# Kernel optimization log

Measured on AMD Instinct MI355X. Metric: run time of the kernel, lower is better.

The kernel has to match this reference:

```python
import jax, jax.numpy as jnp
import numpy as np

H, W = 200, 200           # BEV spatial shape (single level)
NBQ, NH, NL, NP = 2, 8, 1, 4
D = 256
HD = D // NH


def setup_inputs() -> dict:
    key = jax.random.key(0)
    ks = jax.random.split(key, 12)
    bs, nq = 1, H * W
    query = jax.random.normal(ks[0], (bs, nq, D), jnp.float32)
    value = jax.random.normal(ks[1], (bs, NBQ * nq, D), jnp.float32)
    reference_points = jax.random.uniform(ks[2], (bs, nq, NL, 2), dtype=jnp.float32)
    spatial_shapes = jnp.array([[H, W]], dtype=jnp.int32)
    sc = 1.0 / np.sqrt(D)
    W_v = jax.random.normal(ks[3], (D, D), jnp.float32) * sc
    b_v = jax.random.normal(ks[4], (D,), jnp.float32) * 0.01
    W_so = jax.random.normal(ks[5], (2 * D, NBQ * NH * NL * NP * 2), jnp.float32) * 0.02
    b_so = jax.random.normal(ks[6], (NBQ * NH * NL * NP * 2,), jnp.float32) * 0.5
    W_aw = jax.random.normal(ks[7], (2 * D, NBQ * NH * NL * NP), jnp.float32) * 0.02
    b_aw = jax.random.normal(ks[8], (NBQ * NH * NL * NP,), jnp.float32) * 0.01
    W_o = jax.random.normal(ks[9], (D, D), jnp.float32) * sc
    b_o = jax.random.normal(ks[10], (D,), jnp.float32) * 0.01
    return {"query": query, "value": value, "reference_points": reference_points,
            "spatial_shapes": spatial_shapes,
            "W_v": W_v, "b_v": b_v, "W_so": W_so, "b_so": b_so,
            "W_aw": W_aw, "b_aw": b_aw, "W_o": W_o, "b_o": b_o}


def _ms_deform_attn(value, locs, attn):
    # value: (B, K, NH, HD); locs: (B, nq, NH, NL, NP, 2) in [0,1]; attn: (B, nq, NH, NL, NP)
    B, K, h, d = value.shape
    nq = locs.shape[1]
    out = jnp.zeros((B, nq, h, d), value.dtype)
    start = 0
    for l, (Hl, Wl) in enumerate([(H, W)]):
        v = value[:, start:start + Hl * Wl].transpose(0, 2, 1, 3).reshape(B * h, Hl * Wl, d)
        start += Hl * Wl
        g = locs[:, :, :, l]                      # (B, nq, h, NP, 2)
        # grid_sample(align_corners=False, padding='zeros') pixel coords
        x = g[..., 0] * Wl - 0.5
        y = g[..., 1] * Hl - 0.5
        x0 = jnp.floor(x); y0 = jnp.floor(y)
        lx = x - x0; ly = y - y0
        x0 = x0.astype(jnp.int32); y0 = y0.astype(jnp.int32)
        acc = jnp.zeros((B * h, nq * NP, d), value.dtype)
        for dy, wy in ((0, 1.0 - ly), (1, ly)):
            for dx, wx in ((0, 1.0 - lx), (1, lx)):
                xi = x0 + dx; yi = y0 + dy
                valid = ((xi >= 0) & (xi < Wl) & (yi >= 0) & (yi < Hl)).astype(value.dtype)
                idx = jnp.clip(yi, 0, Hl - 1) * Wl + jnp.clip(xi, 0, Wl - 1)  # (B,nq,h,NP)
                idxf = idx.transpose(0, 2, 1, 3).reshape(B * h, nq * NP)
                samp = jnp.take_along_axis(v, idxf[:, :, None], axis=1)       # (B*h, nq*NP, d)
                wgt = (wx * wy * valid).transpose(0, 2, 1, 3).reshape(B * h, nq * NP, 1)
                acc = acc + samp * wgt
        acc = acc.reshape(B, h, nq, NP, d)
        out = out + jnp.einsum('bhqpd,bqhp->bqhd', acc, attn[:, :, :, l])
    return out.reshape(B, nq, h * d)


def reference(query, value, reference_points, spatial_shapes,
              W_v, b_v, W_so, b_so, W_aw, b_aw, W_o, b_o):
    bs, nq, _ = query.shape
    identity = query
    val4 = value.reshape(bs, NBQ, nq, D)
    # query enhanced with most recent bev-queue features
    qe = jnp.concatenate([val4[:, 0], query], axis=-1)           # (bs, nq, 2D)
    vproj = (value @ W_v + b_v).reshape(bs * NBQ, nq, NH, HD)
    off = (qe @ W_so + b_so).reshape(bs, nq, NH, NBQ, NL, NP, 2)
    aw = (qe @ W_aw + b_aw).reshape(bs, nq, NH, NBQ, NL * NP)
    aw = jax.nn.softmax(aw, axis=-1).reshape(bs, nq, NH, NBQ, NL, NP)
    aw = aw.transpose(0, 3, 1, 2, 4, 5).reshape(bs * NBQ, nq, NH, NL, NP)
    # offset normalizer: [W, H] per level
    norm = jnp.stack([spatial_shapes[:, 1], spatial_shapes[:, 0]], -1).astype(query.dtype)  # (NL,2)
    locs = (reference_points[:, :, None, None, :, None, :]
            + off / norm[None, None, None, None, :, None, :])     # (bs,nq,NH,NBQ,NL,NP,2)
    locs = locs.transpose(0, 3, 1, 2, 4, 5, 6).reshape(bs * NBQ, nq, NH, NL, NP, 2)
    out = _ms_deform_attn(vproj, locs, aw)                        # (bs*NBQ, nq, D)
    out = out.reshape(bs, NBQ, nq, D).mean(axis=1)
    return out @ W_o + b_o + identity
```

## Files before the change

### kernel.cpp

```cpp
#include <hip/hip_runtime.h>
#include <math.h>

#define HW_   40000
#define NQ_   40000
#define IMGW  200
#define IMGH  200

typedef __bf16 bf16;
typedef __attribute__((ext_vector_type(4))) __bf16 bf16x4;
typedef __attribute__((ext_vector_type(8))) __bf16 bf16x8;
typedef __attribute__((ext_vector_type(4))) float f32x4;

__device__ __forceinline__ void gload_lds16(const void* g, void* l) {
  __builtin_amdgcn_global_load_lds(
      (const __attribute__((address_space(1))) void*)g,
      (__attribute__((address_space(3))) void*)l, 16, 0, 0);
}

__global__ __launch_bounds__(256) void prep_kernel(
    const float* __restrict__ Wv, const float* __restrict__ Wso,
    const float* __restrict__ Waw, const float* __restrict__ Wo,
    bf16* __restrict__ BtV, bf16* __restrict__ BtOA, bf16* __restrict__ BtO)
{
  int idx = blockIdx.x * 256 + threadIdx.x;
  if (idx < 65536) {
    int k = idx >> 8, n = idx & 255;
    BtV[(size_t)n * 256 + k] = (bf16)Wv[idx];
  } else if (idx < 131072) {
    int j = idx - 65536;
    int k = j >> 7, n = j & 127;
    BtOA[(size_t)n * 512 + k] = (bf16)Wso[j];
  } else if (idx < 163840) {
    int j = idx - 131072;
    int k = j >> 6, n = j & 63;
    BtOA[(size_t)(128 + n) * 512 + k] = (bf16)Waw[j];
  } else if (idx < 229376) {
    int j = idx - 163840;
    int k = j >> 8, n = j & 255;
    BtO[(size_t)n * 256 + k] = (bf16)Wo[j];
  }
}

template<int KT, int MODE, int BN, int AF32>
__global__ __launch_bounds__(256) void mfma_gemm_kernel(
    const void* __restrict__ A0, const void* __restrict__ A1,
    const bf16* __restrict__ Bt,
    const float* __restrict__ bias0, const float* __restrict__ bias1,
    const float* __restrict__ resid,
    void* __restrict__ outp, void* __restrict__ outp2, int M)
{
  constexpr int NT16 = BN / 32;
  constexpr int BCH  = BN / 64;
  constexpr int NIT  = KT / 32;
  __shared__ bf16 As[2][64 * 32];
  __shared__ bf16 Bs[2][BN * 32];
  const int t    = threadIdx.x;
  const int m0   = blockIdx.x * 64;
  const int w    = t >> 6;
  const int lane = t & 63;
  const int quad = lane >> 4;
  const int l16  = lane & 15;
  const int wm   = (w & 1) * 32;
  const int wn   = (w >> 1) * (BN / 2);

  f32x4 acc[2][NT16] = {};

  int gmA;
  {
    int gm = m0 + (t >> 2);
    gmA = (gm >= M) ? (M - 1) : gm;
  }
  const int arow = t >> 2;
  const int akey = (arow >> 1) & 3;

  float4 apf[2];

  auto issueB = [&](int it) {
    const int kt  = it * 32;
    const int buf = it & 1;
#pragma unroll
    for (int i = 0; i < BCH; ++i) {
      int c   = i * 256 + t;
      int row = c >> 2;
      int j   = (c & 3) ^ ((row >> 1) & 3);
      gload_lds16(&Bt[(size_t)row * KT + kt + j * 8], &Bs[buf][c * 8]);
    }
  };

  auto issueA_lds = [&](int it) {
    const int kt  = it * 32;
    const int buf = it & 1;
    const bf16* Ap = (const bf16*)A0;
    int j = (t & 3) ^ akey;
    gload_lds16(&Ap[(size_t)gmA * 256 + kt + j * 8], &As[buf][t * 8]);
  };

  auto loadA_f32 = [&](int it) {
    const int kt = it * 32;
    const float* Ap; int col;
    if (KT == 512) { Ap = (kt < 256) ? (const float*)A0 : (const float*)A1; col = kt & 255; }
    else           { Ap = (const float*)A0; col = kt; }
    const float4* s4 = (const float4*)&Ap[(size_t)gmA * 256 + col + (t & 3) * 8];
    apf[0] = s4[0];
    apf[1] = s4[1];
  };

  auto writeA = [&](int it) {
    const int buf = it & 1;
    int j = (t & 3) ^ akey;
    bf16x8 o = {(bf16)apf[0].x, (bf16)apf[0].y, (bf16)apf[0].z, (bf16)apf[0].w,
                (bf16)apf[1].x, (bf16)apf[1].y, (bf16)apf[1].z, (bf16)apf[1].w};
    *(bf16x8*)&As[buf][arow * 32 + j * 8] = o;
  };

  if (AF32) { loadA_f32(0); issueB(0); writeA(0); }
  else      { issueA_lds(0); issueB(0); }

#pragma unroll
  for (int it = 0; it < NIT; ++it) {
    __syncthreads();
    if (it + 1 < NIT) {
      issueB(it + 1);
      if (AF32) loadA_f32(it + 1); else issueA_lds(it + 1);
    }
    const bf16* as = As[it & 1];
    const bf16* bs = Bs[it & 1];
    bf16x8 af[2], bfr[NT16];
#pragma unroll
    for (int x = 0; x < 2; ++x) {
      int row = wm + x * 16 + l16;
      af[x] = *(const bf16x8*)&as[row * 32 + (quad ^ ((row >> 1) & 3)) * 8];
    }
#pragma unroll
    for (int x = 0; x < NT16; ++x) {
      int row = wn + x * 16 + l16;
      bfr[x] = *(const bf16x8*)&bs[row * 32 + (quad ^ ((row >> 1) & 3)) * 8];
    }
#pragma unroll
    for (int mt = 0; mt < 2; ++mt)
#pragma unroll
      for (int nt = 0; nt < NT16; ++nt)
        acc[mt][nt] = __builtin_amdgcn_mfma_f32_16x16x32_bf16(
            af[mt], bfr[nt], acc[mt][nt], 0, 0, 0);
    if (AF32 && it + 1 < NIT) writeA(it + 1);
  }

#pragma unroll
  for (int mt = 0; mt < 2; ++mt) {
#pragma unroll
    for (int r = 0; r < 4; ++r) {
      const int gm = m0 + wm + mt * 16 + quad * 4 + r;
      if (gm >= M) continue;
#pragma unroll
      for (int nt = 0; nt < NT16; ++nt) {
        const int gn = wn + nt * 16 + l16;
        float v = acc[mt][nt][r];
        if (MODE == 0) {
          int nbq = (gm >= HW_) ? 1 : 0;
          int pix = gm - nbq * HW_;
          int h = gn >> 5, hd = gn & 31;
          ((bf16*)outp)[(((size_t)(nbq * 8 + h) * HW_ + pix) << 5) + hd] =
              (bf16)(v + bias0[gn]);
        } else if (MODE == 1) {
          if (gn < 128)
            ((bf16*)outp)[(size_t)gm * 128 + gn] = (bf16)(v + bias0[gn]);
          else
            ((bf16*)outp2)[(size_t)gm * 64 + (gn - 128)] =
                (bf16)(v + bias1[gn - 128]);
        } else {
          ((float*)outp)[(size_t)gm * 256 + gn] =
              v + bias0[gn] + resid[(size_t)gm * 256 + gn];
        }
      }
    }
  }
}

__global__ __launch_bounds__(256) void deform_attn_kernel(
    const bf16* __restrict__ vws,
    const bf16* __restrict__ off_bf,
    const bf16* __restrict__ aw_bf,
    const float* __restrict__ ref,
    bf16* __restrict__ ms)
{
  const int t    = threadIdx.x;
  const int w    = t >> 6;
  const int lane = t & 63;
  const int h    = blockIdx.x & 7;
  const int qb   = blockIdx.x >> 3;
  const int qi   = lane >> 3;
  const int q    = qb * 32 + w * 8 + qi;
  const int nbq  = (lane >> 2) & 1;
  const int sub  = lane & 3;
  const int g    = h * 2 + nbq;

  const float rx = ref[2 * q + 0] * (float)IMGW - 0.5f;
  const float ry = ref[2 * q + 1] * (float)IMGH - 0.5f;

  bf16x4 a4 = *(const bf16x4*)&aw_bf[(size_t)q * 64 + g * 4];
  float aa0 = (float)a4[0], aa1 = (float)a4[1], aa2 = (float)a4[2], aa3 = (float)a4[3];
  float mx = fmaxf(fmaxf(aa0, aa1), fmaxf(aa2, aa3));
  float e0 = __expf(aa0 - mx), e1 = __expf(aa1 - mx);
  float e2 = __expf(aa2 - mx), e3 = __expf(aa3 - mx);
  float inv = 1.0f / (e0 + e1 + e2 + e3);
  float w4[4] = {e0 * inv, e1 * inv, e2 * inv, e3 * inv};

  bf16x8 o8 = *(const bf16x8*)&off_bf[(size_t)q * 128 + g * 8];
  float ox[4] = {(float)o8[0], (float)o8[2], (float)o8[4], (float)o8[6]};
  float oy[4] = {(float)o8[1], (float)o8[3], (float)o8[5], (float)o8[7]};

  const bf16* vbase = vws + (((size_t)(nbq * 8 + h) * HW_) << 5) + sub * 8;

  float acc[8] = {};
#pragma unroll
  for (int p = 0; p < 4; ++p) {
    float x = rx + ox[p];
    float y = ry + oy[p];
    float xf = floorf(x), yf = floorf(y);
    int   x0 = (int)xf,   y0 = (int)yf;
    float lx = x - xf,    ly = y - yf;
    int   x1 = x0 + 1,    y1 = y0 + 1;
    float w00 = (1.0f - lx) * (1.0f - ly);
    float w01 = lx * (1.0f - ly);
    float w10 = (1.0f - lx) * ly;
    float w11 = lx * ly;
    if (x0 < 0 || x0 >= IMGW) { w00 = 0.0f; w10 = 0.0f; }
    if (x1 < 0 || x1 >= IMGW) { w01 = 0.0f; w11 = 0.0f; }
    if (y0 < 0 || y0 >= IMGH) { w00 = 0.0f; w01 = 0.0f; }
    if (y1 < 0 || y1 >= IMGH) { w10 = 0.0f; w11 = 0.0f; }
    int xc0 = min(max(x0, 0), IMGW - 1), xc1 = min(max(x1, 0), IMGW - 1);
    int yc0 = min(max(y0, 0), IMGH - 1), yc1 = min(max(y1, 0), IMGH - 1);
    bf16x8 v00 = *(const bf16x8*)&vbase[(size_t)(yc0 * IMGW + xc0) << 5];
    bf16x8 v01 = *(const bf16x8*)&vbase[(size_t)(yc0 * IMGW + xc1) << 5];
    bf16x8 v10 = *(const bf16x8*)&vbase[(size_t)(yc1 * IMGW + xc0) << 5];
    bf16x8 v11 = *(const bf16x8*)&vbase[(size_t)(yc1 * IMGW + xc1) << 5];
    float wp = w4[p];
#pragma unroll
    for (int j = 0; j < 8; ++j) {
      float s = w00 * (float)v00[j] + w01 * (float)v01[j] +
                w10 * (float)v10[j] + w11 * (float)v11[j];
      acc[j] = fmaf(wp, s, acc[j]);
    }
  }

#pragma unroll
  for (int j = 0; j < 8; ++j) acc[j] += __shfl_xor(acc[j], 4);

  if (nbq == 0) {
    bf16x8 o;
#pragma unroll
    for (int j = 0; j < 8; ++j) o[j] = (bf16)(0.5f * acc[j]);
    *(bf16x8*)&ms[(size_t)q * 256 + h * 32 + sub * 8] = o;
  }
}

extern "C" void kernel_launch(void* const* d_in, const int* in_sizes, int n_in,
                              void* d_out, int out_size, void* d_ws, size_t ws_size,
                              hipStream_t stream) {
  const float* query = (const float*)d_in[0];
  const float* value = (const float*)d_in[1];
  const float* ref   = (const float*)d_in[2];
  const float* Wv  = (const float*)d_in[4];
  const float* bv  = (const float*)d_in[5];
  const float* Wso = (const float*)d_in[6];
  const float* bso = (const float*)d_in[7];
  const float* Waw = (const float*)d_in[8];
  const float* baw = (const float*)d_in[9];
  const float* Wo  = (const float*)d_in[10];
  const float* bo  = (const float*)d_in[11];
  float* out = (float*)d_out;

  char* p = (char*)d_ws;
  bf16* vws    = (bf16*)p; p += (size_t)2 * 8 * HW_ * 32 * 2;
  bf16* off_bf = (bf16*)p; p += (size_t)NQ_ * 128 * 2;
  bf16* aw_bf  = (bf16*)p; p += (size_t)NQ_ * 64 * 2;
  bf16* ms     = (bf16*)p; p += (size_t)NQ_ * 256 * 2;
  bf16* BtV    = (bf16*)p; p += (size_t)256 * 256 * 2;
  bf16* BtOA   = (bf16*)p; p += (size_t)192 * 512 * 2;
  bf16* BtO    = (bf16*)p; p += (size_t)256 * 256 * 2;

  prep_kernel<<<896, 256, 0, stream>>>(Wv, Wso, Waw, Wo, BtV, BtOA, BtO);

  mfma_gemm_kernel<256, 0, 256, 1><<<1250, 256, 0, stream>>>(
      value, nullptr, BtV, bv, nullptr, nullptr, vws, nullptr, 2 * HW_);
  mfma_gemm_kernel<512, 1, 192, 1><<<625, 256, 0, stream>>>(
      value, query, BtOA, bso, baw, nullptr, off_bf, aw_bf, NQ_);
  deform_attn_kernel<<<10000, 256, 0, stream>>>(vws, off_bf, aw_bf, ref, ms);
  mfma_gemm_kernel<256, 2, 256, 0><<<625, 256, 0, stream>>>(
      ms, nullptr, BtO, bo, nullptr, query, out, nullptr, NQ_);
}
```

Measured before the change: 293.5 us.

## Split deform-attn by queue frame, group-major offsets, defer averaging to output GEMM

The offset/attention-weight GEMM now writes its outputs in a group-major layout, so each deform-attn thread reads one contiguous per-group slice. The deform-attn kernel assigns each block a single queue frame, which removes the cross-lane shuffle and the half-idle store. It also issues all 16 bilinear loads before accumulating, to raise memory-level parallelism. Each frame writes its own bf16 buffer, and the output GEMM loads both buffers and averages them while staging A into LDS. This adds an extra intermediate buffer of write and read traffic and more registers per thread.

```diff
diff --git a/kernel.cpp b/kernel.cpp
--- a/kernel.cpp
+++ b/kernel.cpp
@@ -41,7 +41,7 @@
   }
 }
 
-template<int KT, int MODE, int BN, int AF32>
+template<int KT, int MODE, int BN, int ASRC>
 __global__ __launch_bounds__(256) void mfma_gemm_kernel(
     const void* __restrict__ A0, const void* __restrict__ A1,
     const bf16* __restrict__ Bt,
@@ -74,6 +74,7 @@
   const int akey = (arow >> 1) & 3;
 
   float4 apf[2];
+  bf16x8 ah0, ah1;
 
   auto issueB = [&](int it) {
     const int kt  = it * 32;
@@ -95,25 +96,37 @@
     gload_lds16(&Ap[(size_t)gmA * 256 + kt + j * 8], &As[buf][t * 8]);
   };
 
-  auto loadA_f32 = [&](int it) {
+  auto loadA_reg = [&](int it) {
     const int kt = it * 32;
-    const float* Ap; int col;
-    if (KT == 512) { Ap = (kt < 256) ? (const float*)A0 : (const float*)A1; col = kt & 255; }
-    else           { Ap = (const float*)A0; col = kt; }
-    const float4* s4 = (const float4*)&Ap[(size_t)gmA * 256 + col + (t & 3) * 8];
-    apf[0] = s4[0];
-    apf[1] = s4[1];
+    if (ASRC == 1) {
+      const float* Ap; int col;
+      if (KT == 512) { Ap = (kt < 256) ? (const float*)A0 : (const float*)A1; col = kt & 255; }
+      else           { Ap = (const float*)A0; col = kt; }
+      const float4* s4 = (const float4*)&Ap[(size_t)gmA * 256 + col + (t & 3) * 8];
+      apf[0] = s4[0];
+      apf[1] = s4[1];
+    } else {
+      ah0 = *(const bf16x8*)&((const bf16*)A0)[(size_t)gmA * 256 + kt + (t & 3) * 8];
+      ah1 = *(const bf16x8*)&((const bf16*)A1)[(size_t)gmA * 256 + kt + (t & 3) * 8];
+    }
   };
 
   auto writeA = [&](int it) {
     const int buf = it & 1;
     int j = (t & 3) ^ akey;
-    bf16x8 o = {(bf16)apf[0].x, (bf16)apf[0].y, (bf16)apf[0].z, (bf16)apf[0].w,
-                (bf16)apf[1].x, (bf16)apf[1].y, (bf16)apf[1].z, (bf16)apf[1].w};
+    bf16x8 o;
+    if (ASRC == 1) {
+      o = bf16x8{(bf16)apf[0].x, (bf16)apf[0].y, (bf16)apf[0].z, (bf16)apf[0].w,
+                 (bf16)apf[1].x, (bf16)apf[1].y, (bf16)apf[1].z, (bf16)apf[1].w};
+    } else {
+#pragma unroll
+      for (int e = 0; e < 8; ++e)
+        o[e] = (bf16)(0.5f * ((float)ah0[e] + (float)ah1[e]));
+    }
     *(bf16x8*)&As[buf][arow * 32 + j * 8] = o;
   };
 
-  if (AF32) { loadA_f32(0); issueB(0); writeA(0); }
+  if (ASRC) { loadA_reg(0); issueB(0); writeA(0); }
   else      { issueA_lds(0); issueB(0); }
 
 #pragma unroll
@@ -121,7 +134,7 @@
     __syncthreads();
     if (it + 1 < NIT) {
       issueB(it + 1);
-      if (AF32) loadA_f32(it + 1); else issueA_lds(it + 1);
+      if (ASRC) loadA_reg(it + 1); else issueA_lds(it + 1);
     }
     const bf16* as = As[it & 1];
     const bf16* bs = Bs[it & 1];
@@ -142,7 +155,7 @@
       for (int nt = 0; nt < NT16; ++nt)
         acc[mt][nt] = __builtin_amdgcn_mfma_f32_16x16x32_bf16(
             af[mt], bfr[nt], acc[mt][nt], 0, 0, 0);
-    if (AF32 && it + 1 < NIT) writeA(it + 1);
+    if (ASRC && it + 1 < NIT) writeA(it + 1);
   }
 
 #pragma unroll
@@ -162,11 +175,14 @@
           ((bf16*)outp)[(((size_t)(nbq * 8 + h) * HW_ + pix) << 5) + hd] =
               (bf16)(v + bias0[gn]);
         } else if (MODE == 1) {
-          if (gn < 128)
-            ((bf16*)outp)[(size_t)gm * 128 + gn] = (bf16)(v + bias0[gn]);
-          else
-            ((bf16*)outp2)[(size_t)gm * 64 + (gn - 128)] =
-                (bf16)(v + bias1[gn - 128]);
+          if (gn < 128) {
+            int gg = gn >> 3, e = gn & 7;
+            ((bf16*)outp)[((size_t)gg * NQ_ + gm) * 8 + e] = (bf16)(v + bias0[gn]);
+          } else {
+            int j = gn - 128;
+            int gg = j >> 2, e = j & 3;
+            ((bf16*)outp2)[((size_t)gg * NQ_ + gm) * 4 + e] = (bf16)(v + bias1[j]);
+          }
         } else {
           ((float*)outp)[(size_t)gm * 256 + gn] =
               v + bias0[gn] + resid[(size_t)gm * 256 + gn];
@@ -178,26 +194,30 @@
 
 __global__ __launch_bounds__(256) void deform_attn_kernel(
     const bf16* __restrict__ vws,
-    const bf16* __restrict__ off_bf,
-    const bf16* __restrict__ aw_bf,
+    const bf16* __restrict__ off_g,
+    const bf16* __restrict__ aw_g,
     const float* __restrict__ ref,
-    bf16* __restrict__ ms)
+    bf16* __restrict__ ms0,
+    bf16* __restrict__ ms1)
 {
   const int t    = threadIdx.x;
   const int w    = t >> 6;
   const int lane = t & 63;
-  const int h    = blockIdx.x & 7;
-  const int qb   = blockIdx.x >> 3;
-  const int qi   = lane >> 3;
-  const int q    = qb * 32 + w * 8 + qi;
-  const int nbq  = (lane >> 2) & 1;
+  const int b    = blockIdx.x;
+  const int nbq  = b / 5000;
+  const int bb   = b - nbq * 5000;
+  const int h    = bb & 7;
+  const int qc   = bb >> 3;
+  const int qi   = lane >> 2;
   const int sub  = lane & 3;
+  const int q    = qc * 64 + w * 16 + qi;
   const int g    = h * 2 + nbq;
+  bf16* msN = nbq ? ms1 : ms0;
 
   const float rx = ref[2 * q + 0] * (float)IMGW - 0.5f;
   const float ry = ref[2 * q + 1] * (float)IMGH - 0.5f;
 
-  bf16x4 a4 = *(const bf16x4*)&aw_bf[(size_t)q * 64 + g * 4];
+  bf16x4 a4 = *(const bf16x4*)&aw_g[((size_t)g * NQ_ + q) * 4];
   float aa0 = (float)a4[0], aa1 = (float)a4[1], aa2 = (float)a4[2], aa3 = (float)a4[3];
   float mx = fmaxf(fmaxf(aa0, aa1), fmaxf(aa2, aa3));
   float e0 = __expf(aa0 - mx), e1 = __expf(aa1 - mx);
@@ -205,17 +225,16 @@
   float inv = 1.0f / (e0 + e1 + e2 + e3);
   float w4[4] = {e0 * inv, e1 * inv, e2 * inv, e3 * inv};
 
-  bf16x8 o8 = *(const bf16x8*)&off_bf[(size_t)q * 128 + g * 8];
-  float ox[4] = {(float)o8[0], (float)o8[2], (float)o8[4], (float)o8[6]};
-  float oy[4] = {(float)o8[1], (float)o8[3], (float)o8[5], (float)o8[7]};
+  bf16x8 o8 = *(const bf16x8*)&off_g[((size_t)g * NQ_ + q) * 8];
 
   const bf16* vbase = vws + (((size_t)(nbq * 8 + h) * HW_) << 5) + sub * 8;
 
-  float acc[8] = {};
+  float  ww[16];
+  bf16x8 v[16];
 #pragma unroll
   for (int p = 0; p < 4; ++p) {
-    float x = rx + ox[p];
-    float y = ry + oy[p];
+    float x = rx + (float)o8[2 * p];
+    float y = ry + (float)o8[2 * p + 1];
     float xf = floorf(x), yf = floorf(y);
     int   x0 = (int)xf,   y0 = (int)yf;
     float lx = x - xf,    ly = y - yf;
@@ -230,28 +249,28 @@
     if (y1 < 0 || y1 >= IMGH) { w10 = 0.0f; w11 = 0.0f; }
     int xc0 = min(max(x0, 0), IMGW - 1), xc1 = min(max(x1, 0), IMGW - 1);
     int yc0 = min(max(y0, 0), IMGH - 1), yc1 = min(max(y1, 0), IMGH - 1);
-    bf16x8 v00 = *(const bf16x8*)&vbase[(size_t)(yc0 * IMGW + xc0) << 5];
-    bf16x8 v01 = *(const bf16x8*)&vbase[(size_t)(yc0 * IMGW + xc1) << 5];
-    bf16x8 v10 = *(const bf16x8*)&vbase[(size_t)(yc1 * IMGW + xc0) << 5];
-    bf16x8 v11 = *(const bf16x8*)&vbase[(size_t)(yc1 * IMGW + xc1) << 5];
     float wp = w4[p];
-#pragma unroll
-    for (int j = 0; j < 8; ++j) {
-      float s = w00 * (float)v00[j] + w01 * (float)v01[j] +
-                w10 * (float)v10[j] + w11 * (float)v11[j];
-      acc[j] = fmaf(wp, s, acc[j]);
-    }
-  }
-
-#pragma unroll
-  for (int j = 0; j < 8; ++j) acc[j] += __shfl_xor(acc[j], 4);
-
-  if (nbq == 0) {
-    bf16x8 o;
-#pragma unroll
-    for (int j = 0; j < 8; ++j) o[j] = (bf16)(0.5f * acc[j]);
-    *(bf16x8*)&ms[(size_t)q * 256 + h * 32 + sub * 8] = o;
-  }
+    ww[4 * p + 0] = wp * w00;
+    ww[4 * p + 1] = wp * w01;
+    ww[4 * p + 2] = wp * w10;
+    ww[4 * p + 3] = wp * w11;
+    v[4 * p + 0] = *(const bf16x8*)&vbase[(size_t)(yc0 * IMGW + xc0) << 5];
+    v[4 * p + 1] = *(const bf16x8*)&vbase[(size_t)(yc0 * IMGW + xc1) << 5];
+    v[4 * p + 2] = *(const bf16x8*)&vbase[(size_t)(yc1 * IMGW + xc0) << 5];
+    v[4 * p + 3] = *(const bf16x8*)&vbase[(size_t)(yc1 * IMGW + xc1) << 5];
+  }
+
+  float acc[8] = {};
+#pragma unroll
+  for (int s = 0; s < 16; ++s)
+#pragma unroll
+    for (int j = 0; j < 8; ++j)
+      acc[j] = fmaf(ww[s], (float)v[s][j], acc[j]);
+
+  bf16x8 o;
+#pragma unroll
+  for (int j = 0; j < 8; ++j) o[j] = (bf16)acc[j];
+  *(bf16x8*)&msN[(size_t)q * 256 + h * 32 + sub * 8] = o;
 }
 
 extern "C" void kernel_launch(void* const* d_in, const int* in_sizes, int n_in,
@@ -272,9 +291,10 @@
 
   char* p = (char*)d_ws;
   bf16* vws    = (bf16*)p; p += (size_t)2 * 8 * HW_ * 32 * 2;
-  bf16* off_bf = (bf16*)p; p += (size_t)NQ_ * 128 * 2;
-  bf16* aw_bf  = (bf16*)p; p += (size_t)NQ_ * 64 * 2;
-  bf16* ms     = (bf16*)p; p += (size_t)NQ_ * 256 * 2;
+  bf16* off_g  = (bf16*)p; p += (size_t)16 * NQ_ * 8 * 2;
+  bf16* aw_g   = (bf16*)p; p += (size_t)16 * NQ_ * 4 * 2;
+  bf16* ms0    = (bf16*)p; p += (size_t)NQ_ * 256 * 2;
+  bf16* ms1    = (bf16*)p; p += (size_t)NQ_ * 256 * 2;
   bf16* BtV    = (bf16*)p; p += (size_t)256 * 256 * 2;
   bf16* BtOA   = (bf16*)p; p += (size_t)192 * 512 * 2;
   bf16* BtO    = (bf16*)p; p += (size_t)256 * 256 * 2;
@@ -284,8 +304,8 @@
   mfma_gemm_kernel<256, 0, 256, 1><<<1250, 256, 0, stream>>>(
       value, nullptr, BtV, bv, nullptr, nullptr, vws, nullptr, 2 * HW_);
   mfma_gemm_kernel<512, 1, 192, 1><<<625, 256, 0, stream>>>(
-      value, query, BtOA, bso, baw, nullptr, off_bf, aw_bf, NQ_);
-  deform_attn_kernel<<<10000, 256, 0, stream>>>(vws, off_bf, aw_bf, ref, ms);
-  mfma_gemm_kernel<256, 2, 256, 0><<<625, 256, 0, stream>>>(
-      ms, nullptr, BtO, bo, nullptr, query, out, nullptr, NQ_);
-}
+      value, query, BtOA, bso, baw, nullptr, off_g, aw_g, NQ_);
+  deform_attn_kernel<<<10000, 256, 0, stream>>>(vws, off_g, aw_g, ref, ms0, ms1);
+  mfma_gemm_kernel<256, 2, 256, 2><<<625, 256, 0, stream>>>(
+      ms0, ms1, BtO, bo, nullptr, query, out, nullptr, NQ_);
+}
```

After: 296.3 us. About the same (+1.0%).
